# Kernel tuning notes

Measured on AMD Instinct MI355X. Metric: run time of the kernel, lower is better.

Reference implementation:

```python
import jax, jax.numpy as jnp
import numpy as np

B, S, H = 4, 2048, 768
NUM_HEADS = 12
HEAD_DIM = H // NUM_HEADS


def setup_inputs() -> dict:
    key = jax.random.key(0)
    k1, k2, k3 = jax.random.split(key, 3)
    hidden_states = jax.random.normal(k1, (B, S, H), dtype=jnp.float32)
    # torch Linear weight [out,in]; store transposed [in,out] for x @ W
    w_qkv = jax.random.normal(k2, (H, 3 * H), dtype=jnp.float32) * (1.0 / np.sqrt(H))
    w_out = jax.random.normal(k3, (H, H), dtype=jnp.float32) * (1.0 / np.sqrt(H))
    return {"hidden_states": hidden_states, "w_qkv": w_qkv, "w_out": w_out}


def reference(hidden_states, w_qkv, w_out):
    b, s, h = hidden_states.shape
    qkv = hidden_states @ w_qkv                      # [b,s,3h]
    qkv = qkv.reshape(b, s, 3, NUM_HEADS, HEAD_DIM)
    qkv = jnp.transpose(qkv, (2, 0, 3, 1, 4))        # [3,b,nh,s,hd]
    q, k, v = qkv[0], qkv[1], qkv[2]
    scale = 1.0 / np.sqrt(HEAD_DIM).astype(np.float32)
    scores = jnp.einsum('bhqd,bhkd->bhqk', q, k) * scale   # [b,nh,s,s]
    causal = jnp.triu(jnp.ones((s, s), dtype=bool), k=1)
    scores = jnp.where(causal, jnp.float32(-jnp.inf), scores)
    attn = jax.nn.softmax(scores, axis=-1)
    # dropout is identity in eval mode
    out = jnp.einsum('bhqk,bhkd->bhqd', attn, v)      # [b,nh,s,hd]
    out = jnp.transpose(out, (0, 2, 1, 3)).reshape(b, s, h)
    return out @ w_out
```

## Files before the change

### kernel.cpp

```cpp
#include <hip/hip_runtime.h>
#include <stdint.h>

#define B_ 4
#define S_ 2048
#define H_ 768
#define NH_ 12
#define HD_ 64
#define BH_ (B_ * NH_)

#define QSCALE 0.18033688011112042f

typedef __attribute__((ext_vector_type(4))) float f32x4;
typedef __attribute__((ext_vector_type(16))) float f32x16;
typedef __attribute__((ext_vector_type(8))) __bf16 bf16x8;
typedef __attribute__((ext_vector_type(8))) unsigned short ushort8;

__device__ __forceinline__ unsigned short bf16rne(float f) {
  union { float f; unsigned int u; } v;
  v.f = f;
  unsigned int u = v.u;
  return (unsigned short)((u + 0x7fffu + ((u >> 16) & 1u)) >> 16);
}

#if __has_builtin(__builtin_amdgcn_cvt_pk_bf16_f32)
__device__ __forceinline__ unsigned int pk2(float a, float b) {
  auto r = __builtin_amdgcn_cvt_pk_bf16_f32(a, b);
  return *(unsigned int*)&r;
}
#else
__device__ __forceinline__ unsigned int pk2(float a, float b) {
  return (unsigned int)bf16rne(a) | ((unsigned int)bf16rne(b) << 16);
}
#endif

#if __has_builtin(__builtin_amdgcn_exp2f)
#define EXP2F(x) __builtin_amdgcn_exp2f(x)
#else
#define EXP2F(x) exp2f(x)
#endif

__device__ __forceinline__ void gll16(const void* g, void* l) {
  __builtin_amdgcn_global_load_lds(
      (const __attribute__((address_space(1))) unsigned int*)g,
      (__attribute__((address_space(3))) unsigned int*)l, 16, 0, 0);
}

__device__ __forceinline__ void tconv_body(const float* __restrict__ in,
                                           unsigned short* __restrict__ out,
                                           int R, int C, int bx, int by,
                                           unsigned short (*tile)[72], int tid) {
  int c0 = bx * 64, r0 = by * 64;
#pragma unroll
  for (int i = 0; i < 4; ++i) {
    int c = i * 256 + tid;
    int row = c >> 4, col4 = (c & 15) * 4;
    float4 v = *(const float4*)(in + (size_t)(r0 + row) * C + c0 + col4);
    *(uint2*)(&tile[row][col4]) = (uint2){pk2(v.x, v.y), pk2(v.z, v.w)};
  }
  __syncthreads();
#pragma unroll
  for (int i = 0; i < 2; ++i) {
    int c = i * 256 + tid;
    int oc = c >> 3, r8 = (c & 7) * 8;
    ushort8 v;
#pragma unroll
    for (int j = 0; j < 8; ++j) v[j] = tile[r8 + j][oc];
    *(ushort8*)(out + (size_t)(c0 + oc) * R + r0 + r8) = v;
  }
}

__global__ __launch_bounds__(256) void prep_kernel(const float* __restrict__ hs,
                                                   const float* __restrict__ wqkv,
                                                   const float* __restrict__ wout,
                                                   unsigned short* __restrict__ Xbf,
                                                   unsigned short* __restrict__ Wqkvt,
                                                   unsigned short* __restrict__ Woutt) {
  __shared__ unsigned short tile[64][72];
  int bid = blockIdx.x, tid = threadIdx.x;
  if (bid < 3072) {
    int i = (bid * 256 + tid) * 8;
    const float4* p = (const float4*)(hs + i);
    float4 a = p[0], b = p[1];
    uint4 r = {pk2(a.x, a.y), pk2(a.z, a.w), pk2(b.x, b.y), pk2(b.z, b.w)};
    *(uint4*)(Xbf + i) = r;
  } else if (bid < 3504) {
    int idx = bid - 3072;
    tconv_body(wqkv, Wqkvt, 768, 2304, idx % 36, idx / 36, tile, tid);
  } else {
    int idx = bid - 3504;
    tconv_body(wout, Woutt, 768, 768, idx % 12, idx / 12, tile, tid);
  }
}

template <int MODE>
__device__ __forceinline__ void gemm_core(const unsigned short* __restrict__ A,
                                          const unsigned short* __restrict__ Bm,
                                          void* __restrict__ Cout, int N, int K,
                                          int bm, int bn,
                                          unsigned short* As, unsigned short* Bs) {
  int tid = threadIdx.x;
  int lane = tid & 63, wave = tid >> 6;
  int quad = lane >> 4, l16 = lane & 15;
  int wm = (wave & 1) * 64, wn = (wave >> 1) * 64;
  const unsigned short* Ag = A + (size_t)bm * 128 * K;
  const unsigned short* Bg = Bm + (size_t)bn * 128 * K;

  f32x4 zero = {0.f, 0.f, 0.f, 0.f};
  f32x4 acc[4][4];
#pragma unroll
  for (int mt = 0; mt < 4; ++mt)
#pragma unroll
    for (int nt = 0; nt < 4; ++nt) acc[mt][nt] = zero;

  for (int k0 = 0; k0 < K; k0 += 32) {
#pragma unroll
    for (int i = 0; i < 2; ++i) {
      int c = i * 256 + tid;
      int row = c >> 2, off = (c & 3) * 8;
      gll16(Ag + (size_t)row * K + k0 + off, As + c * 8);
      gll16(Bg + (size_t)row * K + k0 + off, Bs + c * 8);
    }
    __syncthreads();
    bf16x8 af[4], bf[4];
#pragma unroll
    for (int mt = 0; mt < 4; ++mt)
      af[mt] = *(const bf16x8*)(As + (wm + mt * 16 + l16) * 32 + quad * 8);
#pragma unroll
    for (int nt = 0; nt < 4; ++nt)
      bf[nt] = *(const bf16x8*)(Bs + (wn + nt * 16 + l16) * 32 + quad * 8);
#pragma unroll
    for (int mt = 0; mt < 4; ++mt)
#pragma unroll
      for (int nt = 0; nt < 4; ++nt) {
        if (MODE == 2)
          acc[mt][nt] = __builtin_amdgcn_mfma_f32_16x16x32_bf16(af[mt], bf[nt], acc[mt][nt], 0, 0, 0);
        else
          acc[mt][nt] = __builtin_amdgcn_mfma_f32_16x16x32_bf16(bf[nt], af[mt], acc[mt][nt], 0, 0, 0);
      }
    __syncthreads();
  }

  if (MODE == 0) {
    unsigned short* qkv = (unsigned short*)Cout;
    int which = (bn >= 6);
#pragma unroll
    for (int mt = 0; mt < 4; ++mt)
#pragma unroll
      for (int nt = 0; nt < 4; ++nt) {
        int f0 = bn * 128 + wn + nt * 16 + quad * 4;
        int tm = bm * 128 + wm + mt * 16 + l16;
        int rem = f0 - which * 768;
        int head = rem >> 6, d0 = rem & 63;
        int b = tm >> 11, s = tm & 2047;
        if (which == 0) {
          uint2 pkv = {pk2(acc[mt][nt][0] * QSCALE, acc[mt][nt][1] * QSCALE),
                       pk2(acc[mt][nt][2] * QSCALE, acc[mt][nt][3] * QSCALE)};
          *(uint2*)(qkv + (((size_t)b * NH_ + head) * S_ + s) * HD_ + d0) = pkv;
        } else {
          uint2 pkv = {pk2(acc[mt][nt][0], acc[mt][nt][1]),
                       pk2(acc[mt][nt][2], acc[mt][nt][3])};
          int dd0 = (((d0 >> 3) ^ (s & 7)) << 3) | (d0 & 7);
          *(uint2*)(qkv + (((size_t)(BH_ + b * NH_ + head)) * S_ + s) * HD_ + dd0) = pkv;
        }
      }
  } else if (MODE == 2) {
    unsigned short* vt = (unsigned short*)Cout;
#pragma unroll
    for (int mt = 0; mt < 4; ++mt)
#pragma unroll
      for (int nt = 0; nt < 4; ++nt) {
        int f = bn * 128 + wn + nt * 16 + l16;
        int t0 = bm * 128 + wm + mt * 16 + quad * 4;
        int rem = f - 1536;
        int head = rem >> 6, d = rem & 63;
        int b = t0 >> 11, s0 = t0 & 2047;
        int tile = s0 >> 6, sin = s0 & 63;
        int pos = (((sin >> 3) ^ (d & 7)) << 3) | (sin & 7);
        uint2 pkv = {pk2(acc[mt][nt][0], acc[mt][nt][1]),
                     pk2(acc[mt][nt][2], acc[mt][nt][3])};
        *(uint2*)(vt + (((size_t)(b * NH_ + head)) * HD_ + d) * S_ + tile * 64 + pos) = pkv;
      }
  } else {
    float* outp = (float*)Cout;
#pragma unroll
    for (int mt = 0; mt < 4; ++mt)
#pragma unroll
      for (int nt = 0; nt < 4; ++nt) {
        int f0 = bn * 128 + wn + nt * 16 + quad * 4;
        int tm = bm * 128 + wm + mt * 16 + l16;
        *(f32x4*)(outp + (size_t)tm * N + f0) = acc[mt][nt];
      }
  }
}

__global__ __launch_bounds__(256) void gemm_qkv(const unsigned short* __restrict__ A,
                                                const unsigned short* __restrict__ Bm,
                                                unsigned short* __restrict__ QK,
                                                unsigned short* __restrict__ Vt) {
  __shared__ unsigned short As[128 * 32];
  __shared__ unsigned short Bs[128 * 32];
  int bm = blockIdx.x, bn = blockIdx.y;
  if (bn < 12)
    gemm_core<0>(A, Bm, QK, 2304, 768, bm, bn, As, Bs);
  else
    gemm_core<2>(A, Bm, Vt, 2304, 768, bm, bn, As, Bs);
}

__global__ __launch_bounds__(256) void gemm_out(const unsigned short* __restrict__ A,
                                                const unsigned short* __restrict__ Bm,
                                                float* __restrict__ Cout) {
  __shared__ unsigned short As[128 * 32];
  __shared__ unsigned short Bs[128 * 32];
  gemm_core<1>(A, Bm, Cout, 768, 768, blockIdx.x, blockIdx.y, As, Bs);
}

__global__ __launch_bounds__(256, 3) void attn_kernel(const unsigned short* __restrict__ Q,
                                                      const unsigned short* __restrict__ Kg,
                                                      const unsigned short* __restrict__ Vt,
                                                      unsigned short* __restrict__ O) {
  __shared__ unsigned short Ks[2][64 * 64];
  __shared__ unsigned short Vs[2][64 * 64];
  __shared__ unsigned short Ps[4][32 * 64];
  const int pi_[16] = {0, 1, 3, 5, 7, 9, 11, 13, 15, 14, 12, 10, 8, 6, 4, 2};
  int bh = blockIdx.x;
  int y = blockIdx.y;
  int qt = pi_[(bh + y) & 15];
  int tid = threadIdx.x, lane = tid & 63, wave = tid >> 6;
  int l32 = lane & 31, h = lane >> 5;
  const unsigned short* Qp = Q + (size_t)bh * S_ * HD_;
  int q0 = qt * 128;
  int qrow = q0 + wave * 32 + l32;
  int kmax_w = (q0 + wave * 32 + 31) >> 6;
  int kmax_b = 2 * qt + 1;

  const unsigned short* kS = Kg + (size_t)bh * S_ * HD_ + (tid >> 3) * HD_ + (tid & 7) * 8;
  const unsigned short* vS = Vt + (size_t)bh * HD_ * S_ + (size_t)(tid >> 3) * S_ + (tid & 7) * 8;

  auto stage = [&](int t, int buf) {
#pragma unroll
    for (int i = 0; i < 2; ++i) {
      gll16(kS + i * 32 * HD_ + (size_t)t * 4096, &Ks[buf][(i * 256 + tid) * 8]);
      gll16(vS + (size_t)i * 32 * S_ + t * 64, &Vs[buf][(i * 256 + tid) * 8]);
    }
  };

  stage(0, 0);

  bf16x8 qf[4];
#pragma unroll
  for (int dk = 0; dk < 4; ++dk)
    qf[dk] = *(const bf16x8*)(Qp + (size_t)qrow * HD_ + dk * 16 + h * 8);

  bf16x8 ones;
#pragma unroll
  for (int j = 0; j < 8; ++j) ones[j] = (__bf16)1.0f;

  int fo[2][4];
#pragma unroll
  for (int x = 0; x < 2; ++x)
#pragma unroll
    for (int yy = 0; yy < 4; ++yy)
      fo[x][yy] = (x * 32 + l32) * 64 + (((yy * 2 + h) ^ (l32 & 7)) << 3);
  int pwr[2][4];
#pragma unroll
  for (int kb = 0; kb < 2; ++kb)
#pragma unroll
    for (int g = 0; g < 4; ++g)
      pwr[kb][g] = l32 * 64 + ((((kb * 4 + g) ^ (l32 & 7))) << 3) + h * 4;
  unsigned short* psW = &Ps[wave][0];

  f32x16 zero16;
#pragma unroll
  for (int j = 0; j < 16; ++j) zero16[j] = 0.f;
  f32x16 o[2], rsv;
  o[0] = zero16; o[1] = zero16; rsv = zero16;

  auto body = [&](int t, const unsigned short* Kb, const unsigned short* Vb) {
    f32x16 sf[2];
    sf[0] = zero16; sf[1] = zero16;
#pragma unroll
    for (int kb = 0; kb < 2; ++kb)
#pragma unroll
      for (int dk = 0; dk < 4; ++dk) {
        bf16x8 kf = *(const bf16x8*)(Kb + fo[kb][dk]);
        sf[kb] = __builtin_amdgcn_mfma_f32_32x32x16_bf16(kf, qf[dk], sf[kb], 0, 0, 0);
      }

    if (t == kmax_w) {
#pragma unroll
      for (int kb = 0; kb < 2; ++kb)
#pragma unroll
        for (int r = 0; r < 16; ++r)
          if (t * 64 + kb * 32 + (r & 3) + 8 * (r >> 2) + 4 * h > qrow) sf[kb][r] = -1e30f;
    }

#pragma unroll
    for (int kb = 0; kb < 2; ++kb)
#pragma unroll
      for (int g = 0; g < 4; ++g) {
        uint2 pkv = {pk2(EXP2F(sf[kb][g * 4 + 0]), EXP2F(sf[kb][g * 4 + 1])),
                     pk2(EXP2F(sf[kb][g * 4 + 2]), EXP2F(sf[kb][g * 4 + 3]))};
        *(uint2*)(psW + pwr[kb][g]) = pkv;
      }

#pragma unroll
    for (int ks = 0; ks < 4; ++ks) {
      bf16x8 pf = *(const bf16x8*)(psW + fo[0][ks]);
      rsv = __builtin_amdgcn_mfma_f32_32x32x16_bf16(ones, pf, rsv, 0, 0, 0);
#pragma unroll
      for (int db = 0; db < 2; ++db) {
        bf16x8 vf = *(const bf16x8*)(Vb + fo[db][ks]);
        o[db] = __builtin_amdgcn_mfma_f32_32x32x16_bf16(vf, pf, o[db], 0, 0, 0);
      }
    }
  };

  for (int t = 0; t <= kmax_b; t += 2) {
    __syncthreads();
    stage(t + 1, 1);
    if (t <= kmax_w) body(t, &Ks[0][0], &Vs[0][0]);
    __syncthreads();
    if (t + 2 <= kmax_b) stage(t + 2, 0);
    if (t + 1 <= kmax_w) body(t + 1, &Ks[1][0], &Vs[1][0]);
  }

  float inv = 1.f / rsv[0];
  int b = bh / NH_, hh = bh % NH_;
#pragma unroll
  for (int db = 0; db < 2; ++db)
#pragma unroll
    for (int g = 0; g < 4; ++g) {
      uint2 pkv = {pk2(o[db][g * 4 + 0] * inv, o[db][g * 4 + 1] * inv),
                   pk2(o[db][g * 4 + 2] * inv, o[db][g * 4 + 3] * inv)};
      int d0 = db * 32 + 8 * g + 4 * h;
      *(uint2*)(O + ((size_t)b * S_ + qrow) * H_ + hh * HD_ + d0) = pkv;
    }
}

extern "C" void kernel_launch(void* const* d_in, const int* in_sizes, int n_in,
                              void* d_out, int out_size, void* d_ws, size_t ws_size,
                              hipStream_t stream) {
  (void)in_sizes; (void)n_in; (void)out_size; (void)ws_size;
  const float* hs = (const float*)d_in[0];
  const float* wqkv = (const float*)d_in[1];
  const float* wout = (const float*)d_in[2];
  float* out = (float*)d_out;

  unsigned short* Xbf = (unsigned short*)d_ws;
  unsigned short* Wqkvt = Xbf + (size_t)8192 * 768;
  unsigned short* Woutt = Wqkvt + (size_t)2304 * 768;
  unsigned short* QK = Woutt + (size_t)768 * 768;
  unsigned short* Vt = QK + (size_t)2 * BH_ * S_ * HD_;
  unsigned short* Attn = Xbf;

  prep_kernel<<<3648, 256, 0, stream>>>(hs, wqkv, wout, Xbf, Wqkvt, Woutt);
  gemm_qkv<<<dim3(64, 18), 256, 0, stream>>>(Xbf, Wqkvt, QK, Vt);
  attn_kernel<<<dim3(48, 16), 256, 0, stream>>>(QK, QK + (size_t)BH_ * S_ * HD_, Vt, Attn);
  gemm_out<<<dim3(64, 6), 256, 0, stream>>>(Attn, Woutt, out);
}
```

Before: 202.8 us.

## Keep softmax probabilities in registers via permlane swap and pre-tile K/V fragments

The attention kernel no longer round-trips the exponentiated scores through a per-wave LDS buffer. It rearranges the packed bf16 values between lane halves with permlane32_swap to form the B operand of the PV MFMA directly. The QKV GEMM epilogue now writes K and V^T in an MFMA-fragment-ordered tile layout, so staging becomes linear copies and fragment reads are contiguous per lane with no XOR swizzle. Dropping the P buffer frees shared memory, and the occupancy hint rises from 3 to 4 blocks per CU, which may increase register pressure.

```diff
diff --git a/kernel.cpp b/kernel.cpp
--- a/kernel.cpp
+++ b/kernel.cpp
@@ -14,6 +14,8 @@
 typedef __attribute__((ext_vector_type(16))) float f32x16;
 typedef __attribute__((ext_vector_type(8))) __bf16 bf16x8;
 typedef __attribute__((ext_vector_type(8))) unsigned short ushort8;
+typedef __attribute__((ext_vector_type(2))) unsigned int u32x2;
+typedef __attribute__((ext_vector_type(4))) unsigned int u32x4;
 
 __device__ __forceinline__ unsigned short bf16rne(float f) {
   union { float f; unsigned int u; } v;
@@ -37,6 +39,23 @@
 #define EXP2F(x) __builtin_amdgcn_exp2f(x)
 #else
 #define EXP2F(x) exp2f(x)
+#endif
+
+#if __has_builtin(__builtin_amdgcn_permlane32_swap)
+__device__ __forceinline__ u32x2 permswap(unsigned a, unsigned b) {
+  u32x2 r = __builtin_amdgcn_permlane32_swap(a, b, false, false);
+  return r;
+}
+#else
+__device__ __forceinline__ u32x2 permswap(unsigned a, unsigned b) {
+  int l = (int)(threadIdx.x & 63);
+  unsigned ap = (unsigned)__shfl((int)a, l ^ 32, 64);
+  unsigned bp = (unsigned)__shfl((int)b, l ^ 32, 64);
+  u32x2 r;
+  r[0] = (l & 32) ? bp : a;
+  r[1] = (l & 32) ? b : ap;
+  return r;
+}
 #endif
 
 __device__ __forceinline__ void gll16(const void* g, void* l) {
@@ -159,8 +178,10 @@
         } else {
           uint2 pkv = {pk2(acc[mt][nt][0], acc[mt][nt][1]),
                        pk2(acc[mt][nt][2], acc[mt][nt][3])};
-          int dd0 = (((d0 >> 3) ^ (s & 7)) << 3) | (d0 & 7);
-          *(uint2*)(qkv + (((size_t)(BH_ + b * NH_ + head)) * S_ + s) * HD_ + dd0) = pkv;
+          int t = s >> 6, kb = (s >> 5) & 1, row = s & 31;
+          int dk = d0 >> 4, hh = (d0 >> 3) & 1, off = d0 & 7;
+          *(uint2*)(qkv + ((size_t)(BH_ + b * NH_ + head)) * S_ * HD_ + t * 4096
+                    + ((kb * 4 + dk) * 64 + hh * 32 + row) * 8 + off) = pkv;
         }
       }
   } else if (MODE == 2) {
@@ -175,10 +196,12 @@
         int head = rem >> 6, d = rem & 63;
         int b = t0 >> 11, s0 = t0 & 2047;
         int tile = s0 >> 6, sin = s0 & 63;
-        int pos = (((sin >> 3) ^ (d & 7)) << 3) | (sin & 7);
+        int ks = sin >> 4, hh = (sin >> 3) & 1, off = sin & 7;
+        int db = d >> 5, drow = d & 31;
         uint2 pkv = {pk2(acc[mt][nt][0], acc[mt][nt][1]),
                      pk2(acc[mt][nt][2], acc[mt][nt][3])};
-        *(uint2*)(vt + (((size_t)(b * NH_ + head)) * HD_ + d) * S_ + tile * 64 + pos) = pkv;
+        *(uint2*)(vt + ((size_t)(b * NH_ + head)) * HD_ * S_ + tile * 4096
+                  + ((db * 4 + ks) * 64 + hh * 32 + drow) * 8 + off) = pkv;
       }
   } else {
     float* outp = (float*)Cout;
@@ -214,13 +237,12 @@
   gemm_core<1>(A, Bm, Cout, 768, 768, blockIdx.x, blockIdx.y, As, Bs);
 }
 
-__global__ __launch_bounds__(256, 3) void attn_kernel(const unsigned short* __restrict__ Q,
+__global__ __launch_bounds__(256, 4) void attn_kernel(const unsigned short* __restrict__ Q,
                                                       const unsigned short* __restrict__ Kg,
                                                       const unsigned short* __restrict__ Vt,
                                                       unsigned short* __restrict__ O) {
   __shared__ unsigned short Ks[2][64 * 64];
   __shared__ unsigned short Vs[2][64 * 64];
-  __shared__ unsigned short Ps[4][32 * 64];
   const int pi_[16] = {0, 1, 3, 5, 7, 9, 11, 13, 15, 14, 12, 10, 8, 6, 4, 2};
   int bh = blockIdx.x;
   int y = blockIdx.y;
@@ -233,14 +255,15 @@
   int kmax_w = (q0 + wave * 32 + 31) >> 6;
   int kmax_b = 2 * qt + 1;
 
-  const unsigned short* kS = Kg + (size_t)bh * S_ * HD_ + (tid >> 3) * HD_ + (tid & 7) * 8;
-  const unsigned short* vS = Vt + (size_t)bh * HD_ * S_ + (size_t)(tid >> 3) * S_ + (tid & 7) * 8;
+  const unsigned short* kS = Kg + (size_t)bh * S_ * HD_;
+  const unsigned short* vS = Vt + (size_t)bh * HD_ * S_;
 
   auto stage = [&](int t, int buf) {
 #pragma unroll
     for (int i = 0; i < 2; ++i) {
-      gll16(kS + i * 32 * HD_ + (size_t)t * 4096, &Ks[buf][(i * 256 + tid) * 8]);
-      gll16(vS + (size_t)i * 32 * S_ + t * 64, &Vs[buf][(i * 256 + tid) * 8]);
+      int c = (i * 256 + tid) * 8;
+      gll16(kS + (size_t)t * 4096 + c, &Ks[buf][c]);
+      gll16(vS + (size_t)t * 4096 + c, &Vs[buf][c]);
     }
   };
 
@@ -255,19 +278,7 @@
 #pragma unroll
   for (int j = 0; j < 8; ++j) ones[j] = (__bf16)1.0f;
 
-  int fo[2][4];
-#pragma unroll
-  for (int x = 0; x < 2; ++x)
-#pragma unroll
-    for (int yy = 0; yy < 4; ++yy)
-      fo[x][yy] = (x * 32 + l32) * 64 + (((yy * 2 + h) ^ (l32 & 7)) << 3);
-  int pwr[2][4];
-#pragma unroll
-  for (int kb = 0; kb < 2; ++kb)
-#pragma unroll
-    for (int g = 0; g < 4; ++g)
-      pwr[kb][g] = l32 * 64 + ((((kb * 4 + g) ^ (l32 & 7))) << 3) + h * 4;
-  unsigned short* psW = &Ps[wave][0];
+  const int flin = lane * 8;
 
   f32x16 zero16;
 #pragma unroll
@@ -282,7 +293,7 @@
     for (int kb = 0; kb < 2; ++kb)
 #pragma unroll
       for (int dk = 0; dk < 4; ++dk) {
-        bf16x8 kf = *(const bf16x8*)(Kb + fo[kb][dk]);
+        bf16x8 kf = *(const bf16x8*)(Kb + (kb * 4 + dk) * 512 + flin);
         sf[kb] = __builtin_amdgcn_mfma_f32_32x32x16_bf16(kf, qf[dk], sf[kb], 0, 0, 0);
       }
 
@@ -294,22 +305,26 @@
           if (t * 64 + kb * 32 + (r & 3) + 8 * (r >> 2) + 4 * h > qrow) sf[kb][r] = -1e30f;
     }
 
+    unsigned p01[8], p23[8];
 #pragma unroll
     for (int kb = 0; kb < 2; ++kb)
 #pragma unroll
       for (int g = 0; g < 4; ++g) {
-        uint2 pkv = {pk2(EXP2F(sf[kb][g * 4 + 0]), EXP2F(sf[kb][g * 4 + 1])),
-                     pk2(EXP2F(sf[kb][g * 4 + 2]), EXP2F(sf[kb][g * 4 + 3]))};
-        *(uint2*)(psW + pwr[kb][g]) = pkv;
+        p01[kb * 4 + g] = pk2(EXP2F(sf[kb][g * 4 + 0]), EXP2F(sf[kb][g * 4 + 1]));
+        p23[kb * 4 + g] = pk2(EXP2F(sf[kb][g * 4 + 2]), EXP2F(sf[kb][g * 4 + 3]));
       }
 
 #pragma unroll
     for (int ks = 0; ks < 4; ++ks) {
-      bf16x8 pf = *(const bf16x8*)(psW + fo[0][ks]);
+      u32x2 a02 = permswap(p01[2 * ks], p01[2 * ks + 1]);
+      u32x2 a13 = permswap(p23[2 * ks], p23[2 * ks + 1]);
+      u32x4 pu;
+      pu[0] = a02[0]; pu[1] = a13[0]; pu[2] = a02[1]; pu[3] = a13[1];
+      bf16x8 pf = *(bf16x8*)&pu;
       rsv = __builtin_amdgcn_mfma_f32_32x32x16_bf16(ones, pf, rsv, 0, 0, 0);
 #pragma unroll
       for (int db = 0; db < 2; ++db) {
-        bf16x8 vf = *(const bf16x8*)(Vb + fo[db][ks]);
+        bf16x8 vf = *(const bf16x8*)(Vb + (db * 4 + ks) * 512 + flin);
         o[db] = __builtin_amdgcn_mfma_f32_32x32x16_bf16(vf, pf, o[db], 0, 0, 0);
       }
     }
```

New measurement: 198.2 us. 1.02x faster.
